# Kernel optimization log

Measured on AMD Instinct MI355X. Metric: run time of the kernel, lower is better.

## Reference

```python
import jax, jax.numpy as jnp
import numpy as np
import math

D_MODEL = 512; NHEAD = 8; D_HEAD = 64; C_OUT = 64
SEQ_LEN = 1024; PRED_LEN = 256; K = 8; DIM_FF = 2048
LOW_FREQ = 1; EPS = 1e-5
BATCH = 8


def _next_fast_len(n):
    # smallest 5-smooth integer >= n (matches scipy.fftpack.next_fast_len)
    while True:
        m = n
        for p in (2, 3, 5):
            while m % p == 0:
                m //= p
        if m == 1:
            return n
        n += 1


def _conv1d_fft(f, g, n):
    # matches torch conv1d_fft with N == M == n along axis 1 (cross-correlation via conj)
    fast_len = _next_fast_len(2 * n - 1)
    Ff = jnp.fft.rfft(f, n=fast_len, axis=1)
    Fg = jnp.fft.rfft(g, n=fast_len, axis=1)
    out = jnp.fft.irfft(Ff * jnp.conj(Fg), n=fast_len, axis=1)
    out = jnp.roll(out, -1, axis=1)
    return out[:, fast_len - n:fast_len]


def _exp_smooth(values, sw, v0, aux_values=None):
    # values: (b,t,h,d); sw: (h,1); v0: (1,1,h,d or 1)
    b, t, h, d = values.shape
    alpha = jax.nn.sigmoid(sw)                        # (h,1)
    powers = jnp.arange(t, dtype=values.dtype)
    weight = (1.0 - alpha) * alpha ** powers[::-1]    # (h,t)
    init_w = alpha ** (powers + 1.0)                  # (h,t)
    weight = weight.T[None, :, :, None]               # (1,t,h,1)
    init_w = init_w.T[None, :, :, None]
    out = init_w * v0 + _conv1d_fft(values, weight, t)
    if aux_values is not None:
        aux_w = weight * (alpha / (1.0 - alpha))[None, None, :, :]
        out = out + _conv1d_fft(aux_values, aux_w, t)
    return out


def _layer_norm(x, g, b):
    mu = x.mean(-1, keepdims=True)
    var = ((x - mu) ** 2).mean(-1, keepdims=True)
    return (x - mu) * jax.lax.rsqrt(var + EPS) * g + b


def _fourier_season(x):
    b, t, d = x.shape
    xf = jnp.fft.rfft(x, axis=1)                      # (b, t//2+1, d) complex
    hi = xf.shape[1] - 1 if t % 2 == 0 else xf.shape[1]
    xf = xf[:, LOW_FREQ:hi]                           # (b, F, d)
    freqs = (jnp.arange(t // 2 + 1, dtype=x.dtype) / t)[LOW_FREQ:hi]
    # top-K frequencies per (batch, feature) by amplitude
    _, idx = jax.lax.top_k(jnp.abs(jnp.moveaxis(xf, 1, 2)), K)   # (b,d,K)
    idx = jnp.moveaxis(idx, 2, 1)                     # (b,K,d)
    x_sel = jnp.take_along_axis(xf, idx, axis=1)      # (b,K,d) complex
    f_sel = freqs[idx]                                # (b,K,d)
    # trig re-synthesis / extrapolation over t + PRED_LEN steps
    x_all = jnp.concatenate([x_sel, jnp.conj(x_sel)], axis=1)    # (b,2K,d)
    f_all = jnp.concatenate([f_sel, -f_sel], axis=1)[:, :, None, :]  # (b,2K,1,d)
    t_val = jnp.arange(t + PRED_LEN, dtype=x.dtype).reshape(1, 1, -1, 1)
    amp = (jnp.abs(x_all) / t)[:, :, None, :]
    phase = jnp.angle(x_all)[:, :, None, :]
    x_time = amp * jnp.cos(2.0 * math.pi * f_all * t_val + phase)  # (b,2K,T,d)
    return x_time.sum(axis=1)                         # (b, t+PRED_LEN, d)


def _growth_layer(x, z0, in_w, in_b, sw, v0, out_w, out_b):
    b, t, _ = x.shape
    v = (x @ in_w.T + in_b).reshape(b, t, NHEAD, D_HEAD)
    v = jnp.concatenate([jnp.broadcast_to(z0[None, None], (b, 1, NHEAD, D_HEAD)), v], axis=1)
    v = v[:, 1:] - v[:, :-1]                          # first differences, (b,t,h,dh)
    s = _exp_smooth(v, sw, v0)
    s = jnp.concatenate([jnp.broadcast_to(v0, (b, 1, NHEAD, D_HEAD)), s], axis=1)  # (b,t+1,h,dh)
    return s.reshape(b, t + 1, NHEAD * D_HEAD) @ out_w.T + out_b


def _level_layer(level, growth, season, sw, v0, gw, gb, spw, spb):
    b, t, _ = level.shape
    g = (growth @ gw.T + gb)[..., None]               # (b,t,c,1)
    s = (season @ spw.T + spb)[..., None]             # (b,t,c,1)
    l = level[..., None] - s
    out = _exp_smooth(l, sw, v0, aux_values=g)        # (b,t,c,1)
    return out[..., 0]


def _forward(res, level, gl_z0, gl_in_w, gl_in_b, gl_sw, gl_v0, gl_out_w, gl_out_b,
             ll_sw, ll_v0, ll_gw, ll_gb, ll_sw2, ll_sb, ff_w1, ff_w2,
             n1_g, n1_b, n2_g, n2_b):
    season = _fourier_season(res)                     # (b, t+P, d)
    res = res - season[:, :-PRED_LEN]
    growth = _growth_layer(res, gl_z0, gl_in_w, gl_in_b, gl_sw, gl_v0, gl_out_w, gl_out_b)  # (b,t+1,d)
    res = _layer_norm(res - growth[:, 1:], n1_g, n1_b)
    ff = jax.nn.sigmoid(res @ ff_w1.T) @ ff_w2.T      # Feedforward, activation='sigmoid', no bias
    res = _layer_norm(res + ff, n2_g, n2_b)
    level = _level_layer(level, growth[:, :-1], season[:, :-PRED_LEN],
                         ll_sw, ll_v0, ll_gw, ll_gb, ll_sw2, ll_sb)
    return res, level, growth, season


def setup_inputs() -> dict:
    key = jax.random.key(0)
    ks = jax.random.split(key, 16)
    f32 = jnp.float32
    rn = lambda k, shape, s=1.0: jax.random.normal(k, shape, dtype=f32) * s
    return {
        "res": rn(ks[0], (BATCH, SEQ_LEN, D_MODEL)),
        "level": rn(ks[1], (BATCH, SEQ_LEN, C_OUT)),
        "gl_z0": rn(ks[2], (NHEAD, D_HEAD)),
        "gl_in_w": rn(ks[3], (NHEAD * D_HEAD, D_MODEL), 0.02),
        "gl_in_b": jnp.zeros((NHEAD * D_HEAD,), f32),
        "gl_sw": rn(ks[4], (NHEAD, 1)),
        "gl_v0": rn(ks[5], (1, 1, NHEAD, D_HEAD)),
        "gl_out_w": rn(ks[6], (D_MODEL, NHEAD * D_HEAD), 0.02),
        "gl_out_b": jnp.zeros((D_MODEL,), f32),
        "ll_sw": rn(ks[7], (C_OUT, 1)),
        "ll_v0": rn(ks[8], (1, 1, C_OUT, 1)),
        "ll_gw": rn(ks[9], (C_OUT, D_MODEL), 0.02),
        "ll_gb": jnp.zeros((C_OUT,), f32),
        "ll_sw2": rn(ks[10], (C_OUT, D_MODEL), 0.02),
        "ll_sb": jnp.zeros((C_OUT,), f32),
        "ff_w1": rn(ks[11], (DIM_FF, D_MODEL), 0.02),
        "ff_w2": rn(ks[12], (D_MODEL, DIM_FF), 0.02),
        "n1_g": jnp.ones((D_MODEL,), f32),
        "n1_b": jnp.zeros((D_MODEL,), f32),
        "n2_g": jnp.ones((D_MODEL,), f32),
        "n2_b": jnp.zeros((D_MODEL,), f32),
    }


def reference(res, level, gl_z0, gl_in_w, gl_in_b, gl_sw, gl_v0, gl_out_w, gl_out_b,
              ll_sw, ll_v0, ll_gw, ll_gb, ll_sw2, ll_sb, ff_w1, ff_w2,
              n1_g, n1_b, n2_g, n2_b):
    return _forward(res, level, gl_z0, gl_in_w, gl_in_b, gl_sw, gl_v0, gl_out_w, gl_out_b,
                    ll_sw, ll_v0, ll_gw, ll_gb, ll_sw2, ll_sb, ff_w1, ff_w2,
                    n1_g, n1_b, n2_g, n2_b)
```

## Files before the change

### kernel.cpp

```cpp
#include <hip/hip_runtime.h>
#include <hip/hip_bf16.h>
#include <math.h>

#define B_ 8
#define T_ 1024
#define D_ 512
#define PRED 256
#define TP (T_ + PRED)
#define NH 8
#define DH 64
#define DFF 2048
#define CO 64
#define KSEL 8

typedef __hip_bfloat16 bf16;
using bf16x8 = __attribute__((ext_vector_type(8))) short;
using f32x4  = __attribute__((ext_vector_type(4))) float;

__device__ __forceinline__ void gload_lds16(const void* gp, void* lp) {
  __builtin_amdgcn_global_load_lds(
      (const __attribute__((address_space(1))) void*)gp,
      (__attribute__((address_space(3))) void*)lp, 16, 0, 0);
}

template <int N>
__device__ __forceinline__ void vm_wait() {
  if constexpr (N == 0)      asm volatile("s_waitcnt vmcnt(0)" ::: "memory");
  else if constexpr (N == 2) asm volatile("s_waitcnt vmcnt(2)" ::: "memory");
  else if constexpr (N == 4) asm volatile("s_waitcnt vmcnt(4)" ::: "memory");
  else if constexpr (N == 6) asm volatile("s_waitcnt vmcnt(6)" ::: "memory");
  else if constexpr (N == 8) asm volatile("s_waitcnt vmcnt(8)" ::: "memory");
  else static_assert(N == 0, "unsupported vmcnt literal");
}

__global__ __launch_bounds__(256) void k_transpose(const float* __restrict__ in, float* __restrict__ out) {
  __shared__ float tile[32][33];
  const int b = blockIdx.z;
  const int d0 = blockIdx.x * 32, t0 = blockIdx.y * 32;
  const int tx = threadIdx.x, ty = threadIdx.y;
  const float* src = in + ((size_t)b * T_ + t0) * D_ + d0;
#pragma unroll
  for (int i = 0; i < 32; i += 8) tile[ty + i][tx] = src[(size_t)(ty + i) * D_ + tx];
  __syncthreads();
  float* dst = out + ((size_t)b * D_ + d0) * T_ + t0;
#pragma unroll
  for (int i = 0; i < 32; i += 8) dst[(size_t)(ty + i) * T_ + tx] = tile[tx][ty + i];
}

__global__ __launch_bounds__(256) void k_fft_topk(const float* __restrict__ xt, float* __restrict__ comp) {
  __shared__ float2 bufA[2][512], bufB[2][512];
  __shared__ float2 tw[384];
  __shared__ float wvv[2][2][4];
  __shared__ int wkk[2][2][4];
  __shared__ int selk[2][KSEL];
  float* const mg0 = (float*)&bufA[0][0];
  float* const mg1 = (float*)&bufA[1][0];
  const int j = threadIdx.x;
  const size_t bd0 = (size_t)blockIdx.x * 2;
  {
    const float c = -6.283185307179586f / 512.0f;
    tw[j] = make_float2(__cosf(c * (float)j), __sinf(c * (float)j));
    if (j < 128) tw[256 + j] = make_float2(__cosf(c * (float)(256 + j)), __sinf(c * (float)(256 + j)));
  }
  const float4 u0 = ((const float4*)(xt + bd0 * 1024))[j];
  const float4 u1 = ((const float4*)(xt + (bd0 + 1) * 1024))[j];
  bufA[0][2 * j] = make_float2(u0.x, u0.y); bufA[0][2 * j + 1] = make_float2(u0.z, u0.w);
  bufA[1][2 * j] = make_float2(u1.x, u1.y); bufA[1][2 * j + 1] = make_float2(u1.z, u1.w);
  __syncthreads();
  {
    const float2 w = tw[j];
#pragma unroll
    for (int sx2 = 0; sx2 < 2; ++sx2) {
      const float2 a = bufA[sx2][j], b = bufA[sx2][j + 256];
      bufB[sx2][2 * j] = make_float2(a.x + b.x, a.y + b.y);
      const float ex = a.x - b.x, ey = a.y - b.y;
      bufB[sx2][2 * j + 1] = make_float2(ex * w.x - ey * w.y, ex * w.y + ey * w.x);
    }
  }
  __syncthreads();
  const int sx = j >> 7, idx = j & 127;
#pragma unroll
  for (int st = 0; st < 4; ++st) {
    const int lg = 1 + 2 * st;
    const int s = 1 << lg;
    const int p = idx >> lg;
    const int q = idx & (s - 1);
    const float2* src = (st & 1) ? (const float2*)bufA[sx] : (const float2*)bufB[sx];
    float2* dst = (st & 1) ? (float2*)bufB[sx] : (float2*)bufA[sx];
    const float2 x0 = src[idx];
    const float2 x1 = src[idx + 128];
    const float2 x2 = src[idx + 256];
    const float2 x3 = src[idx + 384];
    const float2 e0 = make_float2(x0.x + x2.x, x0.y + x2.y);
    const float2 e1 = make_float2(x0.x - x2.x, x0.y - x2.y);
    const float2 e2 = make_float2(x1.x + x3.x, x1.y + x3.y);
    const float2 e3 = make_float2(x1.x - x3.x, x1.y - x3.y);
    const float2 y0 = make_float2(e0.x + e2.x, e0.y + e2.y);
    const float2 y2 = make_float2(e0.x - e2.x, e0.y - e2.y);
    const float2 y1 = make_float2(e1.x + e3.y, e1.y - e3.x);
    const float2 y3 = make_float2(e1.x - e3.y, e1.y + e3.x);
    const int spi = p << lg;
    const float2 w1 = tw[spi], w2 = tw[2 * spi], w3 = tw[3 * spi];
    const int ob = q + (p << (lg + 2));
    dst[ob] = y0;
    dst[ob + s] = make_float2(y1.x * w1.x - y1.y * w1.y, y1.x * w1.y + y1.y * w1.x);
    dst[ob + 2 * s] = make_float2(y2.x * w2.x - y2.y * w2.y, y2.x * w2.y + y2.y * w2.x);
    dst[ob + 3 * s] = make_float2(y3.x * w3.x - y3.y * w3.y, y3.x * w3.y + y3.y * w3.x);
    __syncthreads();
  }
#pragma unroll
  for (int u = 0; u < 2; ++u) {
    const int k = (u == 0) ? (j + 1) : (j + 257);
    if (k <= 511) {
#pragma unroll
      for (int s2 = 0; s2 < 2; ++s2) {
        const float2 zk = bufB[s2][k & 511];
        const float2 zm = bufB[s2][(512 - k) & 511];
        const float Ex = 0.5f * (zk.x + zm.x), Ey = 0.5f * (zk.y - zm.y);
        const float Ox = 0.5f * (zk.y + zm.y), Oy = 0.5f * (zm.x - zk.x);
        const float ang = -(6.283185307179586f / 1024.0f) * (float)k;
        const float cs = __cosf(ang), sn = __sinf(ang);
        const float Xr = Ex + cs * Ox - sn * Oy;
        const float Xi = Ey + cs * Oy + sn * Ox;
        ((s2 == 0) ? mg0 : mg1)[k] = Xr * Xr + Xi * Xi;
      }
    }
  }
  __syncthreads();
  float a0 = mg0[j], b0v = mg0[j + 256];
  float a1 = mg1[j], b1v = mg1[j + 256];
  if (j == 0) { a0 = -1.0f; a1 = -1.0f; }
  const int lane = j & 63, wvi = j >> 6;
  for (int r = 0; r < KSEL; ++r) {
    const int par = r & 1;
    float bv0 = a0; int bk0 = j;
    if (b0v > bv0) { bv0 = b0v; bk0 = j + 256; }
    float bv1 = a1; int bk1 = j;
    if (b1v > bv1) { bv1 = b1v; bk1 = j + 256; }
#pragma unroll
    for (int off = 32; off; off >>= 1) {
      const float ov0 = __shfl_down(bv0, off); const int ok0 = __shfl_down(bk0, off);
      if (ov0 > bv0 || (ov0 == bv0 && ok0 < bk0)) { bv0 = ov0; bk0 = ok0; }
      const float ov1 = __shfl_down(bv1, off); const int ok1 = __shfl_down(bk1, off);
      if (ov1 > bv1 || (ov1 == bv1 && ok1 < bk1)) { bv1 = ov1; bk1 = ok1; }
    }
    if (lane == 0) {
      wvv[0][par][wvi] = bv0; wkk[0][par][wvi] = bk0;
      wvv[1][par][wvi] = bv1; wkk[1][par][wvi] = bk1;
    }
    __syncthreads();
    float fv0 = wvv[0][par][0]; int fk0 = wkk[0][par][0];
    float fv1 = wvv[1][par][0]; int fk1 = wkk[1][par][0];
#pragma unroll
    for (int i = 1; i < 4; i++) {
      if (wvv[0][par][i] > fv0 || (wvv[0][par][i] == fv0 && wkk[0][par][i] < fk0)) { fv0 = wvv[0][par][i]; fk0 = wkk[0][par][i]; }
      if (wvv[1][par][i] > fv1 || (wvv[1][par][i] == fv1 && wkk[1][par][i] < fk1)) { fv1 = wvv[1][par][i]; fk1 = wkk[1][par][i]; }
    }
    if (j == 0) { selk[0][r] = fk0; selk[1][r] = fk1; }
    if (fk0 == j) a0 = -2.0f;
    if (fk0 == j + 256) b0v = -2.0f;
    if (fk1 == j) a1 = -2.0f;
    if (fk1 == j + 256) b1v = -2.0f;
  }
  __syncthreads();
  if (j < 2 * KSEL) {
    const int s2 = j >> 3, r = j & 7;
    const int k = selk[s2][r];
    const float2 zk = bufB[s2][k & 511];
    const float2 zm = bufB[s2][(512 - k) & 511];
    const float Ex = 0.5f * (zk.x + zm.x), Ey = 0.5f * (zk.y - zm.y);
    const float Ox = 0.5f * (zk.y + zm.y), Oy = 0.5f * (zm.x - zk.x);
    const float ang = -(6.283185307179586f / 1024.0f) * (float)k;
    const float cs = __cosf(ang), sn = __sinf(ang);
    const float Xr = Ex + cs * Ox - sn * Oy;
    const float Xi = Ey + cs * Oy + sn * Ox;
    float* o = comp + (bd0 + s2) * 24 + r * 3;
    o[0] = 2.0f * sqrtf(Xr * Xr + Xi * Xi) * (1.0f / 1024.0f);
    o[1] = (float)k;
    o[2] = atan2f(Xi, Xr);
  }
}

__global__ __launch_bounds__(512) void k_season(const float* __restrict__ comp, const float* __restrict__ res,
                                                float* __restrict__ season, bf16* __restrict__ res1b,
                                                bf16* __restrict__ seasC) {
  const int d = threadIdx.x;
  const int b = blockIdx.y;
  const int t0 = blockIdx.x * 5;
  float a_[8], kf_[8], ph_[8];
  const float* c = comp + ((size_t)b * 512 + d) * 24;
#pragma unroll
  for (int i = 0; i < 8; i++) { a_[i] = c[3 * i]; kf_[i] = c[3 * i + 1]; ph_[i] = c[3 * i + 2]; }
#pragma unroll
  for (int tt = 0; tt < 5; ++tt) {
    const int t = t0 + tt;
    float acc = 0.0f;
#pragma unroll
    for (int i = 0; i < 8; i++) {
      float fr = kf_[i] * (float)t * (1.0f / 1024.0f);
      fr -= floorf(fr);
      acc += a_[i] * __cosf(fmaf(6.283185307179586f, fr, ph_[i]));
    }
    season[((size_t)b * TP + t) * D_ + d] = acc;
    if (t < T_) {
      const float rr = res[((size_t)b * T_ + t) * D_ + d] - acc;
      res1b[((size_t)b * T_ + t) * D_ + d] = __float2bfloat16(rr);
      seasC[((size_t)b * 1025 + t) * 1024 + 512 + d] = __float2bfloat16(acc);
    }
  }
}

#define CVT_TOTAL 2686976
__global__ __launch_bounds__(256) void k_cvt_all(const float* __restrict__ s0, const float* __restrict__ s1,
                                                 const float* __restrict__ s2_, const float* __restrict__ s3,
                                                 const float* __restrict__ s4, const float* __restrict__ s5,
                                                 const float* __restrict__ llsw, bf16* __restrict__ dst) {
  const int i = (blockIdx.x * 256 + threadIdx.x) * 4;
  if (i >= CVT_TOTAL) return;
  const float* src;
  int off;
  float scale = 1.0f;
  int di = i;
  if (i < 262144)       { src = s0;  off = i; }
  else if (i < 524288)  { src = s1;  off = i - 262144; }
  else if (i < 1572864) { src = s2_; off = i - 524288; }
  else if (i < 2621440) { src = s3;  off = i - 1572864; }
  else if (i < 2654208) {
    src = s4;  off = i - 2621440;
    const int c = off >> 9, k = off & 511;
    scale = 1.0f / (1.0f + __expf(-llsw[c]));
    di = 2621440 + c * 1024 + k;
  } else {
    src = s5;  off = i - 2654208;
    const int c = off >> 9, k = off & 511;
    const float alpha = 1.0f / (1.0f + __expf(-llsw[c]));
    scale = -(1.0f - alpha);
    di = 2621440 + c * 1024 + 512 + k;
  }
  const float4 v = *(const float4*)(src + off);
  bf16* o = dst + di;
  o[0] = __float2bfloat16(v.x * scale); o[1] = __float2bfloat16(v.y * scale);
  o[2] = __float2bfloat16(v.z * scale); o[3] = __float2bfloat16(v.w * scale);
}

__global__ __launch_bounds__(1024) void k_growth_scan2(const float* __restrict__ v, const float* __restrict__ z0,
                                                       const float* __restrict__ sw, const float* __restrict__ v0,
                                                       bf16* __restrict__ s2) {
  const int b = blockIdx.x >> 3;
  const int col = (blockIdx.x & 7) * 64 + (threadIdx.x & 63);
  const int w = threadIdx.x >> 6;
  const float alpha = 1.0f / (1.0f + expf(-sw[col >> 6]));
  const float om = 1.0f - alpha;
  float a64 = alpha;
#pragma unroll
  for (int i = 0; i < 6; i++) a64 *= a64;
  const float* vp = v + (size_t)b * T_ * D_ + col;
  float vprev = (w == 0) ? z0[col] : vp[(size_t)(64 * w - 1) * D_];
  float sloc = 0.0f;
#pragma unroll 8
  for (int j = 0; j < 64; j++) {
    const float nv = vp[(size_t)(64 * w + j) * D_];
    sloc = alpha * sloc + om * (nv - vprev);
    vprev = nv;
  }
  __shared__ float lb[16][64], lc[16][64];
  lb[w][threadIdx.x & 63] = sloc;
  __syncthreads();
  if (w == 0) {
    float s = v0[col];
#pragma unroll
    for (int k = 0; k < 16; k++) { lc[k][threadIdx.x & 63] = s; s = a64 * s + lb[k][threadIdx.x & 63]; }
  }
  __syncthreads();
  float s = lc[w][threadIdx.x & 63];
  vprev = (w == 0) ? z0[col] : vp[(size_t)(64 * w - 1) * D_];
  bf16* op = s2 + (size_t)b * (T_ + 1) * D_ + col;
  if (w == 0) op[0] = __float2bfloat16(v0[col]);
#pragma unroll 8
  for (int j = 0; j < 64; j++) {
    const float nv = vp[(size_t)(64 * w + j) * D_];
    s = alpha * s + om * (nv - vprev);
    vprev = nv;
    op[(size_t)(64 * w + j + 1) * D_] = __float2bfloat16(s);
  }
}

__global__ __launch_bounds__(1024) void k_level_scan2(const float* __restrict__ ubuf, const float* __restrict__ sw,
                                                      const float* __restrict__ v0, float* __restrict__ out) {
  const int b = blockIdx.x;
  const int w = threadIdx.x >> 6;
  const int c = threadIdx.x & 63;
  const float alpha = 1.0f / (1.0f + expf(-sw[c]));
  float a64 = alpha;
#pragma unroll
  for (int i = 0; i < 6; i++) a64 *= a64;
  const size_t base = ((size_t)b * T_ + 64 * w) * CO + c;
  float sloc = 0.0f;
#pragma unroll 8
  for (int j = 0; j < 64; j++) sloc = alpha * sloc + ubuf[base + (size_t)j * CO];
  __shared__ float lb[16][64], lc[16][64];
  lb[w][c] = sloc;
  __syncthreads();
  if (w == 0) {
    float s = v0[c];
#pragma unroll
    for (int k = 0; k < 16; k++) { lc[k][c] = s; s = a64 * s + lb[k][c]; }
  }
  __syncthreads();
  float s = lc[w][c];
#pragma unroll 8
  for (int j = 0; j < 64; j++) {
    const size_t idx = base + (size_t)j * CO;
    s = alpha * s + ubuf[idx];
    out[idx] = s;
  }
}

template <int MODE>
__global__ __launch_bounds__(128) void k_ln(const float* __restrict__ x1, const bf16* __restrict__ xb,
                                            const bf16* __restrict__ x3, const float* __restrict__ g,
                                            const float* __restrict__ be, float* __restrict__ outF,
                                            bf16* __restrict__ outB) {
  const int m = blockIdx.x, tid = threadIdx.x;
  const int b = m >> 10;
  float4 v;
  if (MODE == 0) {
    const ushort4 rb = ((const ushort4*)(xb + (size_t)m * D_))[tid];
    const ushort4 gr = ((const ushort4*)(x3 + ((size_t)(m + b + 1)) * 1024))[tid];
    v.x = __uint_as_float((unsigned)rb.x << 16) - __uint_as_float((unsigned)gr.x << 16);
    v.y = __uint_as_float((unsigned)rb.y << 16) - __uint_as_float((unsigned)gr.y << 16);
    v.z = __uint_as_float((unsigned)rb.z << 16) - __uint_as_float((unsigned)gr.z << 16);
    v.w = __uint_as_float((unsigned)rb.w << 16) - __uint_as_float((unsigned)gr.w << 16);
  } else {
    v = ((const float4*)(x1 + (size_t)m * D_))[tid];
  }
  float s = v.x + v.y + v.z + v.w;
  float s2 = v.x * v.x + v.y * v.y + v.z * v.z + v.w * v.w;
#pragma unroll
  for (int off = 32; off; off >>= 1) { s += __shfl_down(s, off); s2 += __shfl_down(s2, off); }
  __shared__ float p1[2], p2[2];
  if ((tid & 63) == 0) { p1[tid >> 6] = s; p2[tid >> 6] = s2; }
  __syncthreads();
  const float S = p1[0] + p1[1], S2 = p2[0] + p2[1];
  const float mu = S * (1.0f / 512.0f);
  const float rs = rsqrtf(fmaxf(S2 * (1.0f / 512.0f) - mu * mu, 0.0f) + 1e-5f);
  const float4 gg = ((const float4*)g)[tid], bb = ((const float4*)be)[tid];
  float4 o;
  o.x = (v.x - mu) * rs * gg.x + bb.x;
  o.y = (v.y - mu) * rs * gg.y + bb.y;
  o.z = (v.z - mu) * rs * gg.z + bb.z;
  o.w = (v.w - mu) * rs * gg.w + bb.w;
  ((float4*)(outF + (size_t)m * D_))[tid] = o;
  if (MODE == 0) {
    bf16* ob = outB + (size_t)m * D_ + tid * 4;
    ob[0] = __float2bfloat16(o.x); ob[1] = __float2bfloat16(o.y);
    ob[2] = __float2bfloat16(o.z); ob[3] = __float2bfloat16(o.w);
  }
}

template <int BM, int BN, int BK, int WM, int WN, int EPI>
__global__ __launch_bounds__(WM * WN * 64, 2) void k_gemm(
    const bf16* __restrict__ A, const bf16* __restrict__ Bw,
    const float* __restrict__ bias, float* outF, bf16* __restrict__ outB,
    const float* resid, const int M, const int N, const int K, const int extra, const int obst,
    const float* __restrict__ sw4, const float* __restrict__ gb4, const float* __restrict__ sb4) {
  constexpr int NW = WM * WN;
  constexpr int FM = BM / (WM * 16);
  constexpr int FN = BN / (WN * 16);
  constexpr int RPC = 512 / BK;
  constexpr int LA = (BM / RPC) / NW, LB = (BN / RPC) / NW;
  constexpr int KK = BK / 32;
  constexpr int TLOADS = LA + LB;
  static_assert(LA >= 1 && LB >= 1, "tile too small for staging split");
  static_assert((BM / RPC) % NW == 0 && (BN / RPC) % NW == 0, "staging split");
  __shared__ bf16 lsA[2][BM * BK];
  __shared__ bf16 lsB[2][BN * BK];
  const int tid = threadIdx.x;
  const int w = tid >> 6, lane = tid & 63;
  const int tm = blockIdx.x, tn = blockIdx.y;
  const int wr = w / WN, wc = w % WN;
  const int r16 = lane & 15, hi = lane >> 4;

  int srowoff, scoloff;
  if constexpr (BK == 64) {
    const int rr = lane >> 3, cs = lane & 7;
    srowoff = rr;
    scoloff = (cs ^ rr) * 8;
  } else {
    const int sr = lane >> 3, cs = lane & 7;
    const int idx = cs ^ (sr & 7);
    srowoff = sr * 2 + (idx >> 2);
    scoloff = (idx & 3) * 8;
  }

  const f32x4 fzero = {0.f, 0.f, 0.f, 0.f};
  f32x4 acc[FM][FN];
#pragma unroll
  for (int i = 0; i < FM; i++)
#pragma unroll
    for (int jj = 0; jj < FN; jj++) acc[i][jj] = fzero;

  const int NT = K / BK;

  auto stage = [&](int kt, int sel) {
#pragma unroll
    for (int q = 0; q < LA; q++) {
      const int g = w * LA + q;
      int m = tm * BM + g * RPC + srowoff;
      if (m > M - 1) m = M - 1;
      m += (m >> 10) * extra;
      gload_lds16(A + (size_t)m * K + (size_t)kt * BK + scoloff, &lsA[sel][g * 512]);
    }
#pragma unroll
    for (int q = 0; q < LB; q++) {
      const int g = w * LB + q;
      const int n = tn * BN + g * RPC + srowoff;
      gload_lds16(Bw + (size_t)n * K + (size_t)kt * BK + scoloff, &lsB[sel][g * 512]);
    }
  };

  auto frag = [&](const bf16* ls, int row, int cc) -> bf16x8 {
    if constexpr (BK == 64) {
      const int g = row >> 3, rr = row & 7;
      return *(const bf16x8*)&ls[g * 512 + rr * 64 + ((cc ^ rr) << 3)];
    } else {
      const int g = row >> 4, rr = row & 15, sr = rr >> 1;
      const int idx = ((rr & 1) << 2) | cc;
      return *(const bf16x8*)&ls[g * 512 + sr * 64 + ((idx ^ (sr & 7)) << 3)];
    }
  };

  stage(0, 0);
  for (int kt = 0; kt < NT; ++kt) {
    const int sel = kt & 1;
    if (kt + 1 < NT) {
      stage(kt + 1, sel ^ 1);
      vm_wait<TLOADS>();
    } else {
      vm_wait<0>();
    }
    __builtin_amdgcn_sched_barrier(0);
    __builtin_amdgcn_s_barrier();
    __builtin_amdgcn_sched_barrier(0);
#pragma unroll
    for (int kk = 0; kk < KK; ++kk) {
      bf16x8 af[FM], bfv[FN];
#pragma unroll
      for (int i = 0; i < FM; i++)
        af[i] = frag(lsA[sel], wr * (FM * 16) + i * 16 + r16, kk * 4 + hi);
#pragma unroll
      for (int jj = 0; jj < FN; jj++)
        bfv[jj] = frag(lsB[sel], wc * (FN * 16) + jj * 16 + r16, kk * 4 + hi);
#pragma unroll
      for (int i = 0; i < FM; i++)
#pragma unroll
        for (int jj = 0; jj < FN; jj++)
          acc[i][jj] = __builtin_amdgcn_mfma_f32_16x16x32_bf16(af[i], bfv[jj], acc[i][jj], 0, 0, 0);
    }
    if (kt + 1 < NT) {
      __builtin_amdgcn_sched_barrier(0);
      __builtin_amdgcn_s_barrier();
      __builtin_amdgcn_sched_barrier(0);
    }
  }

#pragma unroll
  for (int i = 0; i < FM; i++) {
#pragma unroll
    for (int r = 0; r < 4; r++) {
      const int m = tm * BM + wr * (FM * 16) + i * 16 + hi * 4 + r;
      if (m < M) {
#pragma unroll
        for (int jj = 0; jj < FN; jj++) {
          const int n = tn * BN + wc * (FN * 16) + jj * 16 + r16;
          float x = acc[i][jj][r];
          if (bias) x += bias[n];
          const size_t idx = (size_t)m * N + n;
          if (EPI == 0) {
            outF[idx] = x;
          } else if (EPI == 1) {
            outF[idx] = x;
            outB[(size_t)m * obst + n] = __float2bfloat16(x);
          } else if (EPI == 2) {
            outB[(size_t)m * obst + n] = __float2bfloat16(1.0f / (1.0f + __expf(-x)));
          } else if (EPI == 3) {
            outF[idx] = x + resid[idx];
          } else {
            const float a = 1.0f / (1.0f + __expf(-sw4[n]));
            const float om = 1.0f - a;
            outF[idx] = x + a * gb4[n] - om * sb4[n] + om * resid[idx];
          }
        }
      }
    }
  }
}

#define MB (size_t)(1u << 20)
static const size_t OFF_A = 0;
static const size_t OFF_C = 32 * MB;
static const size_t OFF_E = 40 * MB;
static const size_t OFF_F = 46 * MB;
static const size_t OFF_G = 55 * MB;
static const size_t OFF_H = 72 * MB;
static const size_t OFF_J = 88 * MB;
static const size_t OFF_K = 89 * MB;

#define W_IN 0
#define W_OUT 262144
#define W_FF1 524288
#define W_FF2 1572864
#define W_GW 2621440

extern "C" void kernel_launch(void* const* d_in, const int* in_sizes, int n_in, void* d_out, int out_size,
                              void* d_ws, size_t ws_size, hipStream_t stream) {
  (void)in_sizes; (void)n_in; (void)out_size; (void)ws_size;
  const float* res = (const float*)d_in[0];
  const float* level = (const float*)d_in[1];
  const float* gl_z0 = (const float*)d_in[2];
  const float* gl_in_w = (const float*)d_in[3];
  const float* gl_in_b = (const float*)d_in[4];
  const float* gl_sw = (const float*)d_in[5];
  const float* gl_v0 = (const float*)d_in[6];
  const float* gl_out_w = (const float*)d_in[7];
  const float* gl_out_b = (const float*)d_in[8];
  const float* ll_sw = (const float*)d_in[9];
  const float* ll_v0 = (const float*)d_in[10];
  const float* ll_gw = (const float*)d_in[11];
  const float* ll_gb = (const float*)d_in[12];
  const float* ll_sw2 = (const float*)d_in[13];
  const float* ll_sb = (const float*)d_in[14];
  const float* ff_w1 = (const float*)d_in[15];
  const float* ff_w2 = (const float*)d_in[16];
  const float* n1_g = (const float*)d_in[17];
  const float* n1_b = (const float*)d_in[18];
  const float* n2_g = (const float*)d_in[19];
  const float* n2_b = (const float*)d_in[20];

  char* ws = (char*)d_ws;
  float* resT = (float*)(ws + OFF_A);
  float* vbuf = (float*)(ws + OFF_A);
  bf16* hbuf = (bf16*)(ws + OFF_A);
  bf16* res1b = (bf16*)(ws + OFF_C);
  bf16* res2b = (bf16*)(ws + OFF_C);
  bf16* wE = (bf16*)(ws + OFF_E);
  bf16* s2b = (bf16*)(ws + OFF_F);
  bf16* agC = (bf16*)(ws + OFF_G);
  float* res2f = (float*)(ws + OFF_H);
  float* comp = (float*)(ws + OFF_J);
  float* ubuf = (float*)(ws + OFF_K);

  float* o_res = (float*)d_out;
  float* o_level = o_res + 4194304;
  float* o_growth = o_level + 524288;
  float* o_season = o_growth + 4198400;

  k_transpose<<<dim3(16, 32, 8), dim3(32, 8), 0, stream>>>(res, resT);
  k_fft_topk<<<2048, 256, 0, stream>>>(resT, comp);
  k_season<<<dim3(256, 8), 512, 0, stream>>>(comp, res, o_season, res1b, agC);
  k_cvt_all<<<(CVT_TOTAL / 4 + 255) / 256, 256, 0, stream>>>(gl_in_w, gl_out_w, ff_w1, ff_w2, ll_gw, ll_sw2, ll_sw, wE);
  k_gemm<64, 128, 64, 2, 2, 0><<<dim3(128, 4), 256, 0, stream>>>(
      res1b, wE + W_IN, gl_in_b, vbuf, nullptr, nullptr, 8192, 512, 512, 0, 512,
      nullptr, nullptr, nullptr);
  k_growth_scan2<<<64, 1024, 0, stream>>>(vbuf, gl_z0, gl_sw, gl_v0, s2b);
  k_gemm<64, 128, 64, 2, 2, 1><<<dim3(129, 4), 256, 0, stream>>>(
      s2b, wE + W_OUT, gl_out_b, o_growth, agC, nullptr, 8200, 512, 512, 0, 1024,
      nullptr, nullptr, nullptr);
  k_ln<0><<<8192, 128, 0, stream>>>(nullptr, res1b, agC, n1_g, n1_b, res2f, res2b);
  k_gemm<128, 128, 32, 2, 2, 2><<<dim3(64, 16), 256, 0, stream>>>(
      res2b, wE + W_FF1, nullptr, nullptr, hbuf, nullptr, 8192, 2048, 512, 0, 2048,
      nullptr, nullptr, nullptr);
  k_gemm<64, 128, 64, 2, 2, 3><<<dim3(128, 4), 256, 0, stream>>>(
      hbuf, wE + W_FF2, nullptr, res2f, nullptr, res2f, 8192, 512, 2048, 0, 512,
      nullptr, nullptr, nullptr);
  k_ln<1><<<8192, 128, 0, stream>>>(res2f, nullptr, nullptr, n2_g, n2_b, o_res, nullptr);
  k_gemm<64, 64, 64, 4, 1, 4><<<dim3(128, 1), 256, 0, stream>>>(
      agC, wE + W_GW, nullptr, ubuf, nullptr, level, 8192, 64, 1024, 1, 64,
      ll_sw, ll_gb, ll_sb);
  k_level_scan2<<<8, 1024, 0, stream>>>(ubuf, ll_sw, ll_v0, o_level);
}
```

Before: 215.2 us.

## Triple-buffer GEMM K-loop and run FFT top-k with one wavefront per series

The GEMM staging moves from double to triple buffering in LDS, prefetching two K-tiles ahead and waiting on a deeper vmcnt, so global loads have more time to land before use. The FFT/top-k kernel now processes one series per 64-thread block instead of two per 256-thread block. That lets the top-k selection run entirely with wave shuffles and no per-round block barriers or LDS reductions. The cost is more LDS per GEMM block, which may lower occupancy, and more FFT blocks, each with less parallelism.

```diff
diff --git a/kernel.cpp b/kernel.cpp
--- a/kernel.cpp
+++ b/kernel.cpp
@@ -25,11 +25,12 @@
 
 template <int N>
 __device__ __forceinline__ void vm_wait() {
-  if constexpr (N == 0)      asm volatile("s_waitcnt vmcnt(0)" ::: "memory");
-  else if constexpr (N == 2) asm volatile("s_waitcnt vmcnt(2)" ::: "memory");
-  else if constexpr (N == 4) asm volatile("s_waitcnt vmcnt(4)" ::: "memory");
-  else if constexpr (N == 6) asm volatile("s_waitcnt vmcnt(6)" ::: "memory");
-  else if constexpr (N == 8) asm volatile("s_waitcnt vmcnt(8)" ::: "memory");
+  if constexpr (N == 0)       asm volatile("s_waitcnt vmcnt(0)" ::: "memory");
+  else if constexpr (N == 2)  asm volatile("s_waitcnt vmcnt(2)" ::: "memory");
+  else if constexpr (N == 4)  asm volatile("s_waitcnt vmcnt(4)" ::: "memory");
+  else if constexpr (N == 6)  asm volatile("s_waitcnt vmcnt(6)" ::: "memory");
+  else if constexpr (N == 8)  asm volatile("s_waitcnt vmcnt(8)" ::: "memory");
+  else if constexpr (N == 12) asm volatile("s_waitcnt vmcnt(12)" ::: "memory");
   else static_assert(N == 0, "unsupported vmcnt literal");
 }
 
@@ -47,134 +48,124 @@
   for (int i = 0; i < 32; i += 8) dst[(size_t)(ty + i) * T_ + tx] = tile[tx][ty + i];
 }
 
-__global__ __launch_bounds__(256) void k_fft_topk(const float* __restrict__ xt, float* __restrict__ comp) {
-  __shared__ float2 bufA[2][512], bufB[2][512];
-  __shared__ float2 tw[384];
-  __shared__ float wvv[2][2][4];
-  __shared__ int wkk[2][2][4];
-  __shared__ int selk[2][KSEL];
-  float* const mg0 = (float*)&bufA[0][0];
-  float* const mg1 = (float*)&bufA[1][0];
+__global__ __launch_bounds__(64) void k_fft_topk(const float* __restrict__ xt, float* __restrict__ comp) {
+  __shared__ float2 bufA[512], bufB[512], tw[384];
+  float* const mg = (float*)&bufA[0];
   const int j = threadIdx.x;
-  const size_t bd0 = (size_t)blockIdx.x * 2;
+  const size_t bd = blockIdx.x;
   {
     const float c = -6.283185307179586f / 512.0f;
-    tw[j] = make_float2(__cosf(c * (float)j), __sinf(c * (float)j));
-    if (j < 128) tw[256 + j] = make_float2(__cosf(c * (float)(256 + j)), __sinf(c * (float)(256 + j)));
-  }
-  const float4 u0 = ((const float4*)(xt + bd0 * 1024))[j];
-  const float4 u1 = ((const float4*)(xt + (bd0 + 1) * 1024))[j];
-  bufA[0][2 * j] = make_float2(u0.x, u0.y); bufA[0][2 * j + 1] = make_float2(u0.z, u0.w);
-  bufA[1][2 * j] = make_float2(u1.x, u1.y); bufA[1][2 * j + 1] = make_float2(u1.z, u1.w);
-  __syncthreads();
-  {
-    const float2 w = tw[j];
-#pragma unroll
-    for (int sx2 = 0; sx2 < 2; ++sx2) {
-      const float2 a = bufA[sx2][j], b = bufA[sx2][j + 256];
-      bufB[sx2][2 * j] = make_float2(a.x + b.x, a.y + b.y);
-      const float ex = a.x - b.x, ey = a.y - b.y;
-      bufB[sx2][2 * j + 1] = make_float2(ex * w.x - ey * w.y, ex * w.y + ey * w.x);
-    }
-  }
-  __syncthreads();
-  const int sx = j >> 7, idx = j & 127;
+#pragma unroll
+    for (int q = 0; q < 6; q++) {
+      const int i = j + 64 * q;
+      tw[i] = make_float2(__cosf(c * (float)i), __sinf(c * (float)i));
+    }
+  }
+#pragma unroll
+  for (int q = 0; q < 4; q++) {
+    const float4 v = ((const float4*)(xt + bd * 1024))[j + 64 * q];
+    bufA[2 * (j + 64 * q)] = make_float2(v.x, v.y);
+    bufA[2 * (j + 64 * q) + 1] = make_float2(v.z, v.w);
+  }
+  __syncthreads();
+#pragma unroll
+  for (int q = 0; q < 4; q++) {
+    const int p = j + 64 * q;
+    const float2 w = tw[p];
+    const float2 a = bufA[p], b = bufA[p + 256];
+    bufB[2 * p] = make_float2(a.x + b.x, a.y + b.y);
+    const float ex = a.x - b.x, ey = a.y - b.y;
+    bufB[2 * p + 1] = make_float2(ex * w.x - ey * w.y, ex * w.y + ey * w.x);
+  }
+  __syncthreads();
 #pragma unroll
   for (int st = 0; st < 4; ++st) {
     const int lg = 1 + 2 * st;
     const int s = 1 << lg;
-    const int p = idx >> lg;
-    const int q = idx & (s - 1);
-    const float2* src = (st & 1) ? (const float2*)bufA[sx] : (const float2*)bufB[sx];
-    float2* dst = (st & 1) ? (float2*)bufB[sx] : (float2*)bufA[sx];
-    const float2 x0 = src[idx];
-    const float2 x1 = src[idx + 128];
-    const float2 x2 = src[idx + 256];
-    const float2 x3 = src[idx + 384];
-    const float2 e0 = make_float2(x0.x + x2.x, x0.y + x2.y);
-    const float2 e1 = make_float2(x0.x - x2.x, x0.y - x2.y);
-    const float2 e2 = make_float2(x1.x + x3.x, x1.y + x3.y);
-    const float2 e3 = make_float2(x1.x - x3.x, x1.y - x3.y);
-    const float2 y0 = make_float2(e0.x + e2.x, e0.y + e2.y);
-    const float2 y2 = make_float2(e0.x - e2.x, e0.y - e2.y);
-    const float2 y1 = make_float2(e1.x + e3.y, e1.y - e3.x);
-    const float2 y3 = make_float2(e1.x - e3.y, e1.y + e3.x);
-    const int spi = p << lg;
-    const float2 w1 = tw[spi], w2 = tw[2 * spi], w3 = tw[3 * spi];
-    const int ob = q + (p << (lg + 2));
-    dst[ob] = y0;
-    dst[ob + s] = make_float2(y1.x * w1.x - y1.y * w1.y, y1.x * w1.y + y1.y * w1.x);
-    dst[ob + 2 * s] = make_float2(y2.x * w2.x - y2.y * w2.y, y2.x * w2.y + y2.y * w2.x);
-    dst[ob + 3 * s] = make_float2(y3.x * w3.x - y3.y * w3.y, y3.x * w3.y + y3.y * w3.x);
+    const float2* src = (st & 1) ? (const float2*)bufA : (const float2*)bufB;
+    float2* dst = (st & 1) ? (float2*)bufB : (float2*)bufA;
+#pragma unroll
+    for (int h = 0; h < 2; h++) {
+      const int idx = j + 64 * h;
+      const int p = idx >> lg;
+      const int q = idx & (s - 1);
+      const float2 x0 = src[idx];
+      const float2 x1 = src[idx + 128];
+      const float2 x2 = src[idx + 256];
+      const float2 x3 = src[idx + 384];
+      const float2 e0 = make_float2(x0.x + x2.x, x0.y + x2.y);
+      const float2 e1 = make_float2(x0.x - x2.x, x0.y - x2.y);
+      const float2 e2 = make_float2(x1.x + x3.x, x1.y + x3.y);
+      const float2 e3 = make_float2(x1.x - x3.x, x1.y - x3.y);
+      const float2 y0 = make_float2(e0.x + e2.x, e0.y + e2.y);
+      const float2 y2 = make_float2(e0.x - e2.x, e0.y - e2.y);
+      const float2 y1 = make_float2(e1.x + e3.y, e1.y - e3.x);
+      const float2 y3 = make_float2(e1.x - e3.y, e1.y + e3.x);
+      const int spi = p << lg;
+      const float2 w1 = tw[spi], w2 = tw[2 * spi], w3 = tw[3 * spi];
+      const int ob = q + (p << (lg + 2));
+      dst[ob] = y0;
+      dst[ob + s] = make_float2(y1.x * w1.x - y1.y * w1.y, y1.x * w1.y + y1.y * w1.x);
+      dst[ob + 2 * s] = make_float2(y2.x * w2.x - y2.y * w2.y, y2.x * w2.y + y2.y * w2.x);
+      dst[ob + 3 * s] = make_float2(y3.x * w3.x - y3.y * w3.y, y3.x * w3.y + y3.y * w3.x);
+    }
     __syncthreads();
   }
 #pragma unroll
-  for (int u = 0; u < 2; ++u) {
-    const int k = (u == 0) ? (j + 1) : (j + 257);
+  for (int u = 0; u < 8; u++) {
+    const int k = 1 + j + 64 * u;
     if (k <= 511) {
-#pragma unroll
-      for (int s2 = 0; s2 < 2; ++s2) {
-        const float2 zk = bufB[s2][k & 511];
-        const float2 zm = bufB[s2][(512 - k) & 511];
-        const float Ex = 0.5f * (zk.x + zm.x), Ey = 0.5f * (zk.y - zm.y);
-        const float Ox = 0.5f * (zk.y + zm.y), Oy = 0.5f * (zm.x - zk.x);
-        const float ang = -(6.283185307179586f / 1024.0f) * (float)k;
-        const float cs = __cosf(ang), sn = __sinf(ang);
-        const float Xr = Ex + cs * Ox - sn * Oy;
-        const float Xi = Ey + cs * Oy + sn * Ox;
-        ((s2 == 0) ? mg0 : mg1)[k] = Xr * Xr + Xi * Xi;
-      }
-    }
-  }
-  __syncthreads();
-  float a0 = mg0[j], b0v = mg0[j + 256];
-  float a1 = mg1[j], b1v = mg1[j + 256];
-  if (j == 0) { a0 = -1.0f; a1 = -1.0f; }
-  const int lane = j & 63, wvi = j >> 6;
+      const float2 zk = bufB[k];
+      const float2 zm = bufB[(512 - k) & 511];
+      const float Ex = 0.5f * (zk.x + zm.x), Ey = 0.5f * (zk.y - zm.y);
+      const float Ox = 0.5f * (zk.y + zm.y), Oy = 0.5f * (zm.x - zk.x);
+      const float ang = -(6.283185307179586f / 1024.0f) * (float)k;
+      const float cs = __cosf(ang), sn = __sinf(ang);
+      const float Xr = Ex + cs * Ox - sn * Oy;
+      const float Xi = Ey + cs * Oy + sn * Ox;
+      mg[k] = Xr * Xr + Xi * Xi;
+    }
+  }
+  if (j == 0) mg[0] = -1.0f;
+  __syncthreads();
+  float cv[8];
+#pragma unroll
+  for (int u = 0; u < 8; u++) cv[u] = mg[j + 64 * u];
+  int sel[8];
+#pragma unroll
   for (int r = 0; r < KSEL; ++r) {
-    const int par = r & 1;
-    float bv0 = a0; int bk0 = j;
-    if (b0v > bv0) { bv0 = b0v; bk0 = j + 256; }
-    float bv1 = a1; int bk1 = j;
-    if (b1v > bv1) { bv1 = b1v; bk1 = j + 256; }
+    float bv = cv[0];
+    int bu = 0;
+#pragma unroll
+    for (int u = 1; u < 8; u++)
+      if (cv[u] > bv) { bv = cv[u]; bu = u; }
+    int bk = j + 64 * bu;
 #pragma unroll
     for (int off = 32; off; off >>= 1) {
-      const float ov0 = __shfl_down(bv0, off); const int ok0 = __shfl_down(bk0, off);
-      if (ov0 > bv0 || (ov0 == bv0 && ok0 < bk0)) { bv0 = ov0; bk0 = ok0; }
-      const float ov1 = __shfl_down(bv1, off); const int ok1 = __shfl_down(bk1, off);
-      if (ov1 > bv1 || (ov1 == bv1 && ok1 < bk1)) { bv1 = ov1; bk1 = ok1; }
-    }
-    if (lane == 0) {
-      wvv[0][par][wvi] = bv0; wkk[0][par][wvi] = bk0;
-      wvv[1][par][wvi] = bv1; wkk[1][par][wvi] = bk1;
-    }
-    __syncthreads();
-    float fv0 = wvv[0][par][0]; int fk0 = wkk[0][par][0];
-    float fv1 = wvv[1][par][0]; int fk1 = wkk[1][par][0];
-#pragma unroll
-    for (int i = 1; i < 4; i++) {
-      if (wvv[0][par][i] > fv0 || (wvv[0][par][i] == fv0 && wkk[0][par][i] < fk0)) { fv0 = wvv[0][par][i]; fk0 = wkk[0][par][i]; }
-      if (wvv[1][par][i] > fv1 || (wvv[1][par][i] == fv1 && wkk[1][par][i] < fk1)) { fv1 = wvv[1][par][i]; fk1 = wkk[1][par][i]; }
-    }
-    if (j == 0) { selk[0][r] = fk0; selk[1][r] = fk1; }
-    if (fk0 == j) a0 = -2.0f;
-    if (fk0 == j + 256) b0v = -2.0f;
-    if (fk1 == j) a1 = -2.0f;
-    if (fk1 == j + 256) b1v = -2.0f;
-  }
-  __syncthreads();
-  if (j < 2 * KSEL) {
-    const int s2 = j >> 3, r = j & 7;
-    const int k = selk[s2][r];
-    const float2 zk = bufB[s2][k & 511];
-    const float2 zm = bufB[s2][(512 - k) & 511];
+      const float ov = __shfl_down(bv, off);
+      const int ok = __shfl_down(bk, off);
+      if (ov > bv || (ov == bv && ok < bk)) { bv = ov; bk = ok; }
+    }
+    bk = __shfl(bk, 0);
+    sel[r] = bk;
+#pragma unroll
+    for (int u = 0; u < 8; u++)
+      if (bk == j + 64 * u) cv[u] = -2.0f;
+  }
+  if (j < KSEL) {
+    int k = 0;
+#pragma unroll
+    for (int r = 0; r < KSEL; r++)
+      if (j == r) k = sel[r];
+    const float2 zk = bufB[k & 511];
+    const float2 zm = bufB[(512 - k) & 511];
     const float Ex = 0.5f * (zk.x + zm.x), Ey = 0.5f * (zk.y - zm.y);
     const float Ox = 0.5f * (zk.y + zm.y), Oy = 0.5f * (zm.x - zk.x);
     const float ang = -(6.283185307179586f / 1024.0f) * (float)k;
     const float cs = __cosf(ang), sn = __sinf(ang);
     const float Xr = Ex + cs * Ox - sn * Oy;
     const float Xi = Ey + cs * Oy + sn * Ox;
-    float* o = comp + (bd0 + s2) * 24 + r * 3;
+    float* o = comp + bd * 24 + j * 3;
     o[0] = 2.0f * sqrtf(Xr * Xr + Xi * Xi) * (1.0f / 1024.0f);
     o[1] = (float)k;
     o[2] = atan2f(Xi, Xr);
@@ -373,8 +364,8 @@
   constexpr int TLOADS = LA + LB;
   static_assert(LA >= 1 && LB >= 1, "tile too small for staging split");
   static_assert((BM / RPC) % NW == 0 && (BN / RPC) % NW == 0, "staging split");
-  __shared__ bf16 lsA[2][BM * BK];
-  __shared__ bf16 lsB[2][BN * BK];
+  __shared__ bf16 lsA[3][BM * BK];
+  __shared__ bf16 lsB[3][BN * BK];
   const int tid = threadIdx.x;
   const int w = tid >> 6, lane = tid & 63;
   const int tm = blockIdx.x, tn = blockIdx.y;
@@ -431,10 +422,13 @@
   };
 
   stage(0, 0);
+  if (1 < NT) stage(1, 1);
   for (int kt = 0; kt < NT; ++kt) {
-    const int sel = kt & 1;
-    if (kt + 1 < NT) {
-      stage(kt + 1, sel ^ 1);
+    const int sel = kt % 3;
+    if (kt + 2 < NT) {
+      stage(kt + 2, (kt + 2) % 3);
+      vm_wait<2 * TLOADS>();
+    } else if (kt + 1 < NT) {
       vm_wait<TLOADS>();
     } else {
       vm_wait<0>();
@@ -556,7 +550,7 @@
   float* o_season = o_growth + 4198400;
 
   k_transpose<<<dim3(16, 32, 8), dim3(32, 8), 0, stream>>>(res, resT);
-  k_fft_topk<<<2048, 256, 0, stream>>>(resT, comp);
+  k_fft_topk<<<4096, 64, 0, stream>>>(resT, comp);
   k_season<<<dim3(256, 8), 512, 0, stream>>>(comp, res, o_season, res1b, agC);
   k_cvt_all<<<(CVT_TOTAL / 4 + 255) / 256, 256, 0, stream>>>(gl_in_w, gl_out_w, ff_w1, ff_w2, ll_gw, ll_sw2, ll_sw, wE);
   k_gemm<64, 128, 64, 2, 2, 0><<<dim3(128, 4), 256, 0, stream>>>(
```

New measurement: 214.0 us. No clear change (-0.5%).
